# Performance work log

Hardware: AMD Instinct MI355X
Metric: run time of the kernel (lower is better)

The kernel has to match this reference:

```python
import jax, jax.numpy as jnp
import numpy as np

SEQ, EMB, QKV = 4096, 1024, 1024

def setup_inputs() -> dict:
    key = jax.random.key(0)
    k_x, k_q, k_k, k_v = jax.random.split(key, 4)
    scale = 1.0 / np.sqrt(EMB)
    return {
        "x": jax.random.normal(k_x, (SEQ, EMB), dtype=jnp.float32),
        "W_q": jax.random.normal(k_q, (EMB, QKV), dtype=jnp.float32) * scale,
        "W_k": jax.random.normal(k_k, (EMB, QKV), dtype=jnp.float32) * scale,
        "W_v": jax.random.normal(k_v, (EMB, QKV), dtype=jnp.float32) * scale,
    }

def reference(x, W_q, W_k, W_v):
    # Single-head scaled dot-product attention, unbatched: x [S, E]
    d_k = W_q.shape[1]
    Q = x @ W_q          # [S, D]
    K = x @ W_k          # [S, D]
    V = x @ W_v          # [S, D]
    scores = (Q @ K.T) * (1.0 / jnp.sqrt(jnp.asarray(d_k, dtype=x.dtype)))  # [S, S]
    attn = jax.nn.softmax(scores, axis=-1)
    return attn @ V      # [S, D]
```

## Files before the change

### kernel.cpp

```cpp
#include <hip/hip_runtime.h>
#include <cstdint>

#define S_DIM 4096
#define E_DIM 1024
#define D_DIM 1024

typedef __bf16 bf16x8 __attribute__((ext_vector_type(8)));
typedef float  f32x4  __attribute__((ext_vector_type(4)));
typedef unsigned short u16x8 __attribute__((ext_vector_type(8)));

__device__ __forceinline__ unsigned short f2bf(float f) {
  unsigned u = __float_as_uint(f);
  unsigned r = (u + 0x7fffu + ((u >> 16) & 1u)) >> 16;
  return (unsigned short)r;
}

__device__ __forceinline__ void lds_copy16(const unsigned short* g, const unsigned short* l) {
  auto gp = reinterpret_cast<__attribute__((address_space(1))) unsigned int*>(
      reinterpret_cast<uintptr_t>(g));
  auto lp = reinterpret_cast<__attribute__((address_space(3))) unsigned int*>(
      reinterpret_cast<uintptr_t>(l));
  __builtin_amdgcn_global_load_lds(gp, lp, 16, 0, 0);
}

__global__ __launch_bounds__(256) void prep_kernel(
    const float* __restrict__ x,
    const float* __restrict__ Wq, const float* __restrict__ Wk, const float* __restrict__ Wv,
    unsigned short* __restrict__ xbf, unsigned short* __restrict__ Wt,
    float* __restrict__ lsum) {
  const int z = blockIdx.z;
  const int tid = threadIdx.x;
  if (z < 3) {
    const float* W = (z == 0) ? Wq : (z == 1 ? Wk : Wv);
    unsigned short* out = Wt + (size_t)z * E_DIM * D_DIM;
    __shared__ unsigned short tile[32][33];
    int bc = blockIdx.x * 32, br = blockIdx.y * 32;
    int tx = tid & 31, ty = tid >> 5;
#pragma unroll
    for (int i = 0; i < 32; i += 8)
      tile[ty + i][tx] = f2bf(W[(size_t)(br + ty + i) * D_DIM + bc + tx]);
    __syncthreads();
#pragma unroll
    for (int i = 0; i < 32; i += 8)
      out[(size_t)(bc + ty + i) * E_DIM + br + tx] = tile[tx][ty + i];
  } else {
    int bid = blockIdx.y * 32 + blockIdx.x;
    int i = (bid * 256 + tid) * 16;
#pragma unroll
    for (int h = 0; h < 2; h++) {
      float4 a = *(const float4*)(x + i + h * 8);
      float4 b = *(const float4*)(x + i + h * 8 + 4);
      u16x8 o;
      o[0] = f2bf(a.x); o[1] = f2bf(a.y); o[2] = f2bf(a.z); o[3] = f2bf(a.w);
      o[4] = f2bf(b.x); o[5] = f2bf(b.y); o[6] = f2bf(b.z); o[7] = f2bf(b.w);
      *(u16x8*)(xbf + i + h * 8) = o;
    }
    if (bid < 16) lsum[bid * 256 + tid] = 0.f;
  }
}

template <int MODE, int NSPLIT, int BN, int BK>
__device__ __forceinline__ void gemm_body(
    const unsigned short* __restrict__ A, int lda,
    const unsigned short* __restrict__ Bt, int ldb,
    void* __restrict__ Cp, unsigned short* __restrict__ C1, int ldc,
    int Kper, float scale, float* __restrict__ lsum,
    int bm, int bn, unsigned short* sA, unsigned short* sB) {
  constexpr int NF = BN / 32;
  constexpr int NC = BK / 8;
  constexpr int RP = 2048 / BK;
  constexpr int PA = 128 / RP;
  constexpr int PB = BN / RP;
  constexpr int HH = BK / 32;

  const int tid = threadIdx.x;
  const int wave = tid >> 6;
  const int lane = tid & 63;
  const int q    = lane >> 4;
  const int l16  = lane & 15;
  const int lx   = l16 & 7;
  const int wm   = (wave >> 1) * 64;
  const int wn   = (wave & 1) * (BN / 2);

  f32x4 zero = {0.f, 0.f, 0.f, 0.f};
  f32x4 acc[4][NF];
#pragma unroll
  for (int t = 0; t < 4; t++)
#pragma unroll
    for (int u = 0; u < NF; u++) acc[t][u] = zero;

  const int srow   = tid / NC;
  const int schunk = (tid % NC) ^ (srow & 7);
  const unsigned short* ap = A  + (size_t)(bm + srow) * lda + schunk * 8;
  const unsigned short* bp = Bt + (size_t)(bn + srow) * ldb + schunk * 8;
  unsigned short* saw = sA + wave * 512;
  unsigned short* sbw = sB + wave * 512;
  const size_t stepA = (size_t)RP * lda;
  const size_t stepB = (size_t)RP * ldb;

  for (int k0 = 0; k0 < Kper; k0 += BK) {
#pragma unroll
    for (int p = 0; p < PA; p++)
      lds_copy16(ap + k0 + p * stepA, saw + p * 2048);
#pragma unroll
    for (int p = 0; p < PB; p++)
      lds_copy16(bp + k0 + p * stepB, sbw + p * 2048);
    __syncthreads();

#pragma unroll
    for (int h = 0; h < HH; h++) {
      bf16x8 af[4], bfv[NF];
      const int pc = (((h << 2) | q) ^ lx) * 8;
#pragma unroll
      for (int t = 0; t < 4; t++)
        af[t] = *reinterpret_cast<const bf16x8*>(sA + (wm + t * 16 + l16) * BK + pc);
#pragma unroll
      for (int u = 0; u < NF; u++)
        bfv[u] = *reinterpret_cast<const bf16x8*>(sB + (wn + u * 16 + l16) * BK + pc);
#pragma unroll
      for (int t = 0; t < 4; t++)
#pragma unroll
        for (int u = 0; u < NF; u++)
          acc[t][u] = __builtin_amdgcn_mfma_f32_16x16x32_bf16(af[t], bfv[u], acc[t][u], 0, 0, 0);
    }
    __syncthreads();
  }

  unsigned short* cb16 = (unsigned short*)Cp;
  int coloff = bn;
  if constexpr (NSPLIT == 2) {
    if (bn >= 1024) cb16 = C1;
    coloff = bn & 1023;
  }
  float* o32 = (float*)Cp;

#pragma unroll
  for (int t = 0; t < 4; t++) {
#pragma unroll
    for (int rr = 0; rr < 4; rr++) {
      const int row = bm + wm + t * 16 + q * 4 + rr;
      float invl = 1.0f;
      if constexpr (MODE == 2) invl = 1.0f / lsum[row];
      float rs = 0.f;
#pragma unroll
      for (int u = 0; u < NF; u++) {
        const int col = coloff + wn + u * 16 + l16;
        float v = acc[t][u][rr] * scale;
        if constexpr (MODE == 0) {
          cb16[(size_t)row * ldc + col] = f2bf(v);
        } else if constexpr (MODE == 1) {
          float p = __expf(v - 8.0f);
          rs += p;
          cb16[(size_t)row * ldc + col] = f2bf(p);
        } else {
          o32[(size_t)row * ldc + col] = acc[t][u][rr] * invl;
        }
      }
      if constexpr (MODE == 1) {
        rs += __shfl_xor(rs, 1);
        rs += __shfl_xor(rs, 2);
        rs += __shfl_xor(rs, 4);
        rs += __shfl_xor(rs, 8);
        if (l16 == 0) unsafeAtomicAdd(&lsum[row], rs);
      }
    }
  }
}

__global__ __launch_bounds__(256, 2) void qk_gemm(
    const unsigned short* __restrict__ xbf, const unsigned short* __restrict__ Wt,
    unsigned short* __restrict__ Qbf, unsigned short* __restrict__ Kbf) {
  __shared__ __align__(16) unsigned short sA[128 * 64];
  __shared__ __align__(16) unsigned short sB[128 * 64];
  const int bid = blockIdx.x;
  const int g = bid >> 7, r = bid & 127;
  gemm_body<0, 2, 128, 64>(xbf, E_DIM, Wt, E_DIM, Qbf, Kbf, D_DIM,
                           E_DIM, 1.0f, nullptr,
                           (g * 8 + (r & 7)) * 128, (r >> 3) * 128, sA, sB);
}

__global__ __launch_bounds__(256, 2) void sv_gemm(
    const unsigned short* __restrict__ xbf, const unsigned short* __restrict__ Wt,
    const unsigned short* __restrict__ Qbf, const unsigned short* __restrict__ Kbf,
    unsigned short* __restrict__ Vt, unsigned short* __restrict__ SP,
    float* __restrict__ lsum) {
  __shared__ __align__(16) unsigned short sA[128 * 64];
  __shared__ __align__(16) unsigned short sB[128 * 64];
  const int bid = blockIdx.x;
  if (bid < 256) {
    gemm_body<0, 1, 128, 64>(Wt + 2 * E_DIM * D_DIM, E_DIM, xbf, E_DIM, Vt,
                             nullptr, S_DIM, E_DIM, 1.0f, nullptr,
                             (bid & 7) * 128, (bid >> 3) * 128, sA, sB);
  } else {
    const int idx = bid - 256;
    const int g = idx >> 8, r = idx & 255;
    gemm_body<1, 1, 128, 64>(Qbf, D_DIM, Kbf, D_DIM, SP, nullptr, S_DIM,
                             D_DIM, 0.03125f, lsum,
                             (g * 8 + (r & 7)) * 128, (r >> 3) * 128, sA, sB);
  }
}

__global__ __launch_bounds__(256, 2) void o_gemm(
    const unsigned short* __restrict__ SP, const unsigned short* __restrict__ Vt,
    float* __restrict__ out, const float* __restrict__ lsum) {
  __shared__ __align__(16) unsigned short sA[128 * 128];
  __shared__ __align__(16) unsigned short sB[64 * 128];
  int flat = blockIdx.y * gridDim.x + blockIdx.x;
  int numInG = 8 * gridDim.x;
  int g = flat / numInG;
  int r = flat - g * numInG;
  int bm = (g * 8 + (r & 7)) * 128, bn = (r >> 3) * 64;
  gemm_body<2, 1, 64, 128>(SP, S_DIM, Vt, S_DIM, out, nullptr, D_DIM,
                           S_DIM, 1.0f, (float*)lsum, bm, bn, sA, sB);
}

extern "C" void kernel_launch(void* const* d_in, const int* in_sizes, int n_in,
                              void* d_out, int out_size, void* d_ws, size_t ws_size,
                              hipStream_t stream) {
  const float* x  = (const float*)d_in[0];
  const float* Wq = (const float*)d_in[1];
  const float* Wk = (const float*)d_in[2];
  const float* Wv = (const float*)d_in[3];
  float* out = (float*)d_out;

  char* ws = (char*)d_ws;
  const size_t MB = 1024 * 1024;
  unsigned short* SP   = (unsigned short*)(ws);
  unsigned short* xbf  = (unsigned short*)(ws + 8 * MB);
  unsigned short* Wt   = (unsigned short*)(ws + 16 * MB);
  unsigned short* Qbf  = (unsigned short*)(ws + 32 * MB);
  unsigned short* Kbf  = (unsigned short*)(ws + 40 * MB);
  unsigned short* Vt   = (unsigned short*)(ws + 48 * MB);
  float*          lsum = (float*)(ws + 56 * MB);

  dim3 blk(256);

  dim3 prgrid(32, 32, 4);
  prep_kernel<<<prgrid, blk, 0, stream>>>(x, Wq, Wk, Wv, xbf, Wt, lsum);

  qk_gemm<<<dim3(512), blk, 0, stream>>>(xbf, Wt, Qbf, Kbf);

  sv_gemm<<<dim3(1280), blk, 0, stream>>>(xbf, Wt, Qbf, Kbf, Vt, SP, lsum);

  dim3 ogrid(16, 32);
  o_gemm<<<ogrid, blk, 0, stream>>>(SP, Vt, out, lsum);
}
```

Baseline: 204.1 us.

## Double-buffer LDS tiles with counted vmcnt waits in QK and SV GEMMs

Adds a DBUF template path to the shared GEMM body. While the current K-tile is being computed, the next tile's global-to-LDS DMA is issued into a second buffer, and a counted s_waitcnt vmcnt(8) waits only for the older stage. The goal is to overlap memory latency with MFMA work in the qk and sv kernels, which doubles their LDS usage to 64KB per block and may limit occupancy. The o_gemm kernel keeps the single-buffer path, and the counted wait relies on exactly eight DMAs per stage.

```diff
diff --git a/kernel.cpp b/kernel.cpp
--- a/kernel.cpp
+++ b/kernel.cpp
@@ -59,7 +59,7 @@
   }
 }
 
-template <int MODE, int NSPLIT, int BN, int BK>
+template <int MODE, int NSPLIT, int BN, int BK, bool DBUF>
 __device__ __forceinline__ void gemm_body(
     const unsigned short* __restrict__ A, int lda,
     const unsigned short* __restrict__ Bt, int ldb,
@@ -72,6 +72,9 @@
   constexpr int PA = 128 / RP;
   constexpr int PB = BN / RP;
   constexpr int HH = BK / 32;
+  constexpr int ABUF = 128 * BK;
+  constexpr int BBUF = BN * BK;
+  static_assert(!DBUF || (PA + PB) == 8, "counted vmcnt(8) assumes 8 DMAs/stage");
 
   const int tid = threadIdx.x;
   const int wave = tid >> 6;
@@ -93,37 +96,65 @@
   const int schunk = (tid % NC) ^ (srow & 7);
   const unsigned short* ap = A  + (size_t)(bm + srow) * lda + schunk * 8;
   const unsigned short* bp = Bt + (size_t)(bn + srow) * ldb + schunk * 8;
-  unsigned short* saw = sA + wave * 512;
-  unsigned short* sbw = sB + wave * 512;
+  const int so = tid * 8 - (tid & 511) * 8 + (tid & 511) * 8;
   const size_t stepA = (size_t)RP * lda;
   const size_t stepB = (size_t)RP * ldb;
 
-  for (int k0 = 0; k0 < Kper; k0 += BK) {
-#pragma unroll
-    for (int p = 0; p < PA; p++)
-      lds_copy16(ap + k0 + p * stepA, saw + p * 2048);
-#pragma unroll
-    for (int p = 0; p < PB; p++)
-      lds_copy16(bp + k0 + p * stepB, sbw + p * 2048);
-    __syncthreads();
-
+  auto stage = [&](int kt, int buf) {
+    const unsigned short* a = ap + (size_t)kt * BK;
+    const unsigned short* b = bp + (size_t)kt * BK;
+    unsigned short* da = sA + buf * ABUF + wave * 512;
+    unsigned short* db = sB + buf * BBUF + wave * 512;
+#pragma unroll
+    for (int p = 0; p < PA; p++) lds_copy16(a + p * stepA, da + p * 2048);
+#pragma unroll
+    for (int p = 0; p < PB; p++) lds_copy16(b + p * stepB, db + p * 2048);
+  };
+
+  auto compute = [&](int buf) {
+    const unsigned short* la = sA + buf * ABUF;
+    const unsigned short* lb = sB + buf * BBUF;
 #pragma unroll
     for (int h = 0; h < HH; h++) {
       bf16x8 af[4], bfv[NF];
       const int pc = (((h << 2) | q) ^ lx) * 8;
 #pragma unroll
       for (int t = 0; t < 4; t++)
-        af[t] = *reinterpret_cast<const bf16x8*>(sA + (wm + t * 16 + l16) * BK + pc);
+        af[t] = *reinterpret_cast<const bf16x8*>(la + (wm + t * 16 + l16) * BK + pc);
 #pragma unroll
       for (int u = 0; u < NF; u++)
-        bfv[u] = *reinterpret_cast<const bf16x8*>(sB + (wn + u * 16 + l16) * BK + pc);
+        bfv[u] = *reinterpret_cast<const bf16x8*>(lb + (wn + u * 16 + l16) * BK + pc);
 #pragma unroll
       for (int t = 0; t < 4; t++)
 #pragma unroll
         for (int u = 0; u < NF; u++)
           acc[t][u] = __builtin_amdgcn_mfma_f32_16x16x32_bf16(af[t], bfv[u], acc[t][u], 0, 0, 0);
     }
-    __syncthreads();
+  };
+
+  if constexpr (DBUF) {
+    const int NT = Kper / BK;
+    stage(0, 0);
+#pragma unroll 1
+    for (int t = 0; t < NT; ++t) {
+      const int b = t & 1;
+      if (t + 1 < NT) {
+        stage(t + 1, b ^ 1);
+        asm volatile("s_waitcnt vmcnt(8)" ::: "memory");
+      } else {
+        asm volatile("s_waitcnt vmcnt(0)" ::: "memory");
+      }
+      asm volatile("s_barrier" ::: "memory");
+      compute(b);
+      asm volatile("s_barrier" ::: "memory");
+    }
+  } else {
+    for (int k0 = 0; k0 < Kper; k0 += BK) {
+      stage(k0 / BK, 0);
+      __syncthreads();
+      compute(0);
+      __syncthreads();
+    }
   }
 
   unsigned short* cb16 = (unsigned short*)Cp;
@@ -170,13 +201,13 @@
 __global__ __launch_bounds__(256, 2) void qk_gemm(
     const unsigned short* __restrict__ xbf, const unsigned short* __restrict__ Wt,
     unsigned short* __restrict__ Qbf, unsigned short* __restrict__ Kbf) {
-  __shared__ __align__(16) unsigned short sA[128 * 64];
-  __shared__ __align__(16) unsigned short sB[128 * 64];
+  __shared__ __align__(16) unsigned short sA[2 * 128 * 64];
+  __shared__ __align__(16) unsigned short sB[2 * 128 * 64];
   const int bid = blockIdx.x;
   const int g = bid >> 7, r = bid & 127;
-  gemm_body<0, 2, 128, 64>(xbf, E_DIM, Wt, E_DIM, Qbf, Kbf, D_DIM,
-                           E_DIM, 1.0f, nullptr,
-                           (g * 8 + (r & 7)) * 128, (r >> 3) * 128, sA, sB);
+  gemm_body<0, 2, 128, 64, true>(xbf, E_DIM, Wt, E_DIM, Qbf, Kbf, D_DIM,
+                                 E_DIM, 1.0f, nullptr,
+                                 (g * 8 + (r & 7)) * 128, (r >> 3) * 128, sA, sB);
 }
 
 __global__ __launch_bounds__(256, 2) void sv_gemm(
@@ -184,19 +215,19 @@
     const unsigned short* __restrict__ Qbf, const unsigned short* __restrict__ Kbf,
     unsigned short* __restrict__ Vt, unsigned short* __restrict__ SP,
     float* __restrict__ lsum) {
-  __shared__ __align__(16) unsigned short sA[128 * 64];
-  __shared__ __align__(16) unsigned short sB[128 * 64];
+  __shared__ __align__(16) unsigned short sA[2 * 128 * 64];
+  __shared__ __align__(16) unsigned short sB[2 * 128 * 64];
   const int bid = blockIdx.x;
   if (bid < 256) {
-    gemm_body<0, 1, 128, 64>(Wt + 2 * E_DIM * D_DIM, E_DIM, xbf, E_DIM, Vt,
-                             nullptr, S_DIM, E_DIM, 1.0f, nullptr,
-                             (bid & 7) * 128, (bid >> 3) * 128, sA, sB);
+    gemm_body<0, 1, 128, 64, true>(Wt + 2 * E_DIM * D_DIM, E_DIM, xbf, E_DIM, Vt,
+                                   nullptr, S_DIM, E_DIM, 1.0f, nullptr,
+                                   (bid & 7) * 128, (bid >> 3) * 128, sA, sB);
   } else {
     const int idx = bid - 256;
     const int g = idx >> 8, r = idx & 255;
-    gemm_body<1, 1, 128, 64>(Qbf, D_DIM, Kbf, D_DIM, SP, nullptr, S_DIM,
-                             D_DIM, 0.03125f, lsum,
-                             (g * 8 + (r & 7)) * 128, (r >> 3) * 128, sA, sB);
+    gemm_body<1, 1, 128, 64, true>(Qbf, D_DIM, Kbf, D_DIM, SP, nullptr, S_DIM,
+                                   D_DIM, 0.03125f, lsum,
+                                   (g * 8 + (r & 7)) * 128, (r >> 3) * 128, sA, sB);
   }
 }
 
@@ -210,8 +241,8 @@
   int g = flat / numInG;
   int r = flat - g * numInG;
   int bm = (g * 8 + (r & 7)) * 128, bn = (r >> 3) * 64;
-  gemm_body<2, 1, 64, 128>(SP, S_DIM, Vt, S_DIM, out, nullptr, D_DIM,
-                           S_DIM, 1.0f, (float*)lsum, bm, bn, sA, sB);
+  gemm_body<2, 1, 64, 128, false>(SP, S_DIM, Vt, S_DIM, out, nullptr, D_DIM,
+                                  S_DIM, 1.0f, (float*)lsum, bm, bn, sA, sB);
 }
 
 extern "C" void kernel_launch(void* const* d_in, const int* in_sizes, int n_in,
```

New measurement: 208.4 us. 2.1% more time.

## Remap GEMM tiles per XCD and widen prep transpose tiles

Applied to the files above, without the earlier changes.

Block indices in the QK, V and score GEMMs are remapped so that blocks landing on the same XCD (bid & 7 round-robin) share A rows and B columns, aiming to raise per-XCD L2 reuse. The prep kernel's weight transpose moves to 64x64 tiles with 8-byte vectorized stores. The x-to-bf16 conversion now handles four chunks per block, so the prep grid shrinks to 16x16x4. The mapping assumes round-robin dispatch across eight XCDs, and the new transposed LDS writes may hit bank conflicts.

```diff
diff --git a/kernel.cpp b/kernel.cpp
--- a/kernel.cpp
+++ b/kernel.cpp
@@ -33,27 +33,33 @@
   if (z < 3) {
     const float* W = (z == 0) ? Wq : (z == 1 ? Wk : Wv);
     unsigned short* out = Wt + (size_t)z * E_DIM * D_DIM;
-    __shared__ unsigned short tile[32][33];
-    int bc = blockIdx.x * 32, br = blockIdx.y * 32;
-    int tx = tid & 31, ty = tid >> 5;
-#pragma unroll
-    for (int i = 0; i < 32; i += 8)
-      tile[ty + i][tx] = f2bf(W[(size_t)(br + ty + i) * D_DIM + bc + tx]);
+    __shared__ unsigned short tile[64][68];
+    const int bc = blockIdx.x * 64;
+    const int br = blockIdx.y * 64;
+    const int tx = tid & 63, ty = tid >> 6;
+#pragma unroll
+    for (int i = 0; i < 64; i += 4)
+      tile[tx][ty + i] = f2bf(W[(size_t)(br + ty + i) * D_DIM + bc + tx]);
     __syncthreads();
-#pragma unroll
-    for (int i = 0; i < 32; i += 8)
-      out[(size_t)(bc + ty + i) * E_DIM + br + tx] = tile[tx][ty + i];
+    const int dr = tid >> 4, eg = tid & 15;
+#pragma unroll
+    for (int i = 0; i < 64; i += 16)
+      *(unsigned long long*)(out + (size_t)(bc + dr + i) * E_DIM + br + eg * 4) =
+          *(const unsigned long long*)(&tile[dr + i][eg * 4]);
   } else {
-    int bid = blockIdx.y * 32 + blockIdx.x;
-    int i = (bid * 256 + tid) * 16;
-#pragma unroll
-    for (int h = 0; h < 2; h++) {
-      float4 a = *(const float4*)(x + i + h * 8);
-      float4 b = *(const float4*)(x + i + h * 8 + 4);
-      u16x8 o;
-      o[0] = f2bf(a.x); o[1] = f2bf(a.y); o[2] = f2bf(a.z); o[3] = f2bf(a.w);
-      o[4] = f2bf(b.x); o[5] = f2bf(b.y); o[6] = f2bf(b.z); o[7] = f2bf(b.w);
-      *(u16x8*)(xbf + i + h * 8) = o;
+    int bid = blockIdx.y * 16 + blockIdx.x;
+#pragma unroll
+    for (int s = 0; s < 4; ++s) {
+      int i = ((bid * 4 + s) * 256 + tid) * 16;
+#pragma unroll
+      for (int h = 0; h < 2; h++) {
+        float4 a = *(const float4*)(x + i + h * 8);
+        float4 b = *(const float4*)(x + i + h * 8 + 4);
+        u16x8 o;
+        o[0] = f2bf(a.x); o[1] = f2bf(a.y); o[2] = f2bf(a.z); o[3] = f2bf(a.w);
+        o[4] = f2bf(b.x); o[5] = f2bf(b.y); o[6] = f2bf(b.z); o[7] = f2bf(b.w);
+        *(u16x8*)(xbf + i + h * 8) = o;
+      }
     }
     if (bid < 16) lsum[bid * 256 + tid] = 0.f;
   }
@@ -173,10 +179,11 @@
   __shared__ __align__(16) unsigned short sA[128 * 64];
   __shared__ __align__(16) unsigned short sB[128 * 64];
   const int bid = blockIdx.x;
-  const int g = bid >> 7, r = bid & 127;
+  const int xcd = bid & 7, j = bid >> 3;
+  const int bm = ((xcd & 3) * 8 + (j >> 3)) * 128;
+  const int bn = ((xcd >> 2) * 8 + (j & 7)) * 128;
   gemm_body<0, 2, 128, 64>(xbf, E_DIM, Wt, E_DIM, Qbf, Kbf, D_DIM,
-                           E_DIM, 1.0f, nullptr,
-                           (g * 8 + (r & 7)) * 128, (r >> 3) * 128, sA, sB);
+                           E_DIM, 1.0f, nullptr, bm, bn, sA, sB);
 }
 
 __global__ __launch_bounds__(256, 2) void sv_gemm(
@@ -188,15 +195,18 @@
   __shared__ __align__(16) unsigned short sB[128 * 64];
   const int bid = blockIdx.x;
   if (bid < 256) {
+    const int xcd = bid & 7, j = bid >> 3;
+    const int bm = (j & 7) * 128;
+    const int bn = (xcd * 4 + (j >> 3)) * 128;
     gemm_body<0, 1, 128, 64>(Wt + 2 * E_DIM * D_DIM, E_DIM, xbf, E_DIM, Vt,
-                             nullptr, S_DIM, E_DIM, 1.0f, nullptr,
-                             (bid & 7) * 128, (bid >> 3) * 128, sA, sB);
+                             nullptr, S_DIM, E_DIM, 1.0f, nullptr, bm, bn, sA, sB);
   } else {
     const int idx = bid - 256;
-    const int g = idx >> 8, r = idx & 255;
+    const int xcd = idx & 7, j = idx >> 3;
+    const int bm = ((xcd & 1) * 16 + (j >> 3)) * 128;
+    const int bn = ((xcd >> 1) * 8 + (j & 7)) * 128;
     gemm_body<1, 1, 128, 64>(Qbf, D_DIM, Kbf, D_DIM, SP, nullptr, S_DIM,
-                             D_DIM, 0.03125f, lsum,
-                             (g * 8 + (r & 7)) * 128, (r >> 3) * 128, sA, sB);
+                             D_DIM, 0.03125f, lsum, bm, bn, sA, sB);
   }
 }
 
@@ -235,7 +245,7 @@
 
   dim3 blk(256);
 
-  dim3 prgrid(32, 32, 4);
+  dim3 prgrid(16, 16, 4);
   prep_kernel<<<prgrid, blk, 0, stream>>>(x, Wq, Wk, Wv, xbf, Wt, lsum);
 
   qk_gemm<<<dim3(512), blk, 0, stream>>>(xbf, Wt, Qbf, Kbf);
```

Result: faster. 199.3 us (-2.3%).
